# Optimization experiments

Hardware: AMD Instinct MI355X
Metric: run time of the kernel (lower is better)

Reference implementation:

```python
import jax, jax.numpy as jnp
import numpy as np

# Config matching init_kwargs
DIM = 768; NH = 12; K = 16; BASE_LR = 1.0  # mini_batch_size K, ttt_base_lr


def _ln(x, g, b, eps=1e-6):
    mu = x.mean(-1, keepdims=True)
    var = x.var(-1, keepdims=True)
    return g * (x - mu) * jax.lax.rsqrt(var + eps) + b


def _ln_l2_bwd(x, tgt, g, b, eps=1e-6):
    # grad wrt x of ||LN(x; g, b) - tgt||^2 (TTT fused layernorm-l2 backward)
    D = x.shape[-1]
    mu = x.mean(-1, keepdims=True)
    var = x.var(-1, keepdims=True)
    std = jnp.sqrt(var + eps)
    xh = (x - mu) / std
    gout = (g * xh + b) - tgt
    gxh = gout * g
    return (D * gxh - gxh.sum(-1, keepdims=True) - xh * (gxh * xh).sum(-1, keepdims=True)) / (D * std)


def _rotary(x, fc):
    # x: [..., N, hd]; fc: [N, hd//2] complex
    xr = x.reshape(*x.shape[:-1], -1, 2)
    xc = jax.lax.complex(xr[..., 0], xr[..., 1]) * fc
    return jnp.stack([jnp.real(xc), jnp.imag(xc)], -1).reshape(x.shape)


def setup_inputs() -> dict:
    key = jax.random.key(0)
    ks = jax.random.split(key, 6)
    B, N, C = 16, 1024, DIM
    nh2, hd, W2 = 2 * NH, C // NH, 2 * C
    f = jnp.float32
    x = jax.random.normal(ks[0], (B, N, C), f)
    qkv_w = jax.random.normal(ks[1], (C, 3 * C), f) * (1.0 / np.sqrt(C))
    proj_w = jax.random.normal(ks[2], (C, C), f) * (1.0 / np.sqrt(C))
    proj_b = jnp.zeros((C,), f)
    W1 = jax.random.normal(ks[3], (nh2, hd, hd), f) * 0.02  # per-head fast-weight init
    b1 = jnp.zeros((nh2, 1, hd), f)
    ttt_ln_w = jnp.ones((nh2, hd), f)
    ttt_ln_b = jnp.zeros((nh2, hd), f)
    post_ln_w = jnp.ones((W2,), f)
    post_ln_b = jnp.zeros((W2,), f)
    lr_w = jax.random.normal(ks[4], (W2, nh2), f) * 0.02  # learnable ttt lr projection
    lr_b = jnp.zeros((nh2,), f)
    token_idx_delta = jnp.zeros((K,), f)  # learnable token-idx offset, init 0
    return dict(x=x, qkv_w=qkv_w, proj_w=proj_w, proj_b=proj_b, W1=W1, b1=b1,
                ttt_ln_w=ttt_ln_w, ttt_ln_b=ttt_ln_b, post_ln_w=post_ln_w, post_ln_b=post_ln_b,
                lr_w=lr_w, lr_b=lr_b, token_idx_delta=token_idx_delta)


def reference(x, qkv_w, proj_w, proj_b, W1, b1, ttt_ln_w, ttt_ln_b,
              post_ln_w, post_ln_b, lr_w, lr_b, token_idx_delta):
    B, N, C = x.shape
    nh2, hd, W2 = 2 * NH, C // NH, 2 * C
    nmb = N // K
    # fused QKV projection (no bias)
    q, k, v = jnp.split(x @ qkv_w, 3, axis=-1)  # each [B,N,C]
    # bidirectional: concat forward stream with token-flipped backward stream
    qq = jnp.concatenate([q, jnp.flip(q, axis=-2)], axis=-1)  # [B,N,2C]
    kk = jnp.concatenate([k, jnp.flip(k, axis=-2)], axis=-1)
    vv = jnp.concatenate([v, jnp.flip(v, axis=-2)], axis=-1)
    xx = jnp.concatenate([x, jnp.flip(x, axis=-2)], axis=-1)

    def heads(t):  # [B,N,2C] -> [B,nh2,N,hd]
        return t.reshape(B, N, nh2, hd).transpose(0, 2, 1, 3)
    XQ, XK, XV = heads(qq), heads(kk), heads(vv)

    # rotary embedding with position_ids % mini_batch_size
    pos = (jnp.arange(N) % K).astype(jnp.float32)
    inv = 1.0 / (10000.0 ** (jnp.arange(0, hd, 2, dtype=jnp.float32) / hd))
    ang = pos[:, None] * inv[None, :]
    fc = jax.lax.complex(jnp.cos(ang), jnp.sin(ang))  # [N, hd//2]
    XQ = _rotary(XQ, fc)
    XK = _rotary(XK, fc)

    def mb(t):  # [B,nh2,N,hd] -> [B,nh2,nmb,K,hd]
        return t.reshape(B, nh2, nmb, K, hd)
    XQ, XK, XV = mb(XQ), mb(XK), mb(XV)

    # eta: token_idx (1/i, learnable offset, clipped) x per-token learnable lr
    Xr = xx.reshape(B, nmb, K, W2)
    lr = jax.nn.sigmoid(Xr @ lr_w + lr_b) * (BASE_LR / hd)  # [B,nmb,K,nh2]
    tok = jnp.clip(1.0 / jnp.arange(1, K + 1, dtype=jnp.float32) + token_idx_delta, 0.0)
    # eta[b,h,m,i,j] = tok[i] * lr[b,m,j,h]
    eta = tok[None, None, None, :, None] * lr.transpose(0, 3, 1, 2)[:, :, :, None, :]  # [B,nh2,nmb,K,K]

    mask = jnp.tril(jnp.ones((K, K), x.dtype))  # AR mask within mini-batch
    g = ttt_ln_w[None, :, None, :]   # [1,nh2,1,hd]
    bt = ttt_ln_b[None, :, None, :]
    W1_0 = jnp.broadcast_to(W1[None], (B, nh2, hd, hd))
    b1_0 = jnp.broadcast_to(b1[None], (B, nh2, 1, hd))

    def step(carry, inp):
        W, bb = carry
        xq, xk, xv, et = inp  # [B,nh2,K,hd] x3, [B,nh2,K,K]
        Z1 = xk @ W + bb
        grad = _ln_l2_bwd(Z1, xv - xk, g, bt)  # dl/dZ1
        attn = jnp.einsum('bhid,bhjd->bhij', xq, xk) * mask
        b1_bar = bb - (et * mask) @ grad
        Z1_bar = xq @ W - (et * attn) @ grad + b1_bar
        last = et[..., -1, :, None]  # eta row of last token [B,nh2,K,1]
        Wn = W - jnp.einsum('bhkd,bhke->bhde', last * xk, grad)
        bn = bb - (last * grad).sum(-2, keepdims=True)
        out = xq + _ln(Z1_bar, g, bt)  # residual + per-head TTT layernorm
        return (Wn, bn), out

    xs = (XQ.transpose(2, 0, 1, 3, 4), XK.transpose(2, 0, 1, 3, 4),
          XV.transpose(2, 0, 1, 3, 4), eta.transpose(2, 0, 1, 3, 4))
    _, Z = jax.lax.scan(step, (W1_0, b1_0), xs)  # Z: [nmb,B,nh2,K,hd]

    Z = Z.transpose(1, 2, 0, 3, 4).reshape(B, nh2, N, hd).transpose(0, 2, 1, 3).reshape(B, N, W2)
    Z = _ln(Z, post_ln_w, post_ln_b)  # mult_norm post-norm
    zf, zb = jnp.split(Z, 2, axis=-1)
    out = zf * jnp.flip(zb, axis=-2)  # merge forward / flipped-backward streams
    return out @ proj_w + proj_b
```

## Files before the change

kernel.cpp:

```cpp
#include <hip/hip_runtime.h>
#include <hip/hip_bf16.h>

#define Bq   16
#define Nseq 1024
#define Cdim 768
#define NH2  24
#define W2D  1536
#define KB   16
#define NMB  64

typedef short bfrag8 __attribute__((ext_vector_type(8)));
typedef short bfrag4 __attribute__((ext_vector_type(4)));
typedef float f32x4  __attribute__((ext_vector_type(4)));

__device__ __forceinline__ short f2bs(float x) {
  union { __hip_bfloat16 b; short s; } u;
  u.b = __float2bfloat16(x);
  return u.s;
}
__device__ __forceinline__ bfrag8 cvt8(const float* v) {
  bfrag8 r;
#pragma unroll
  for (int i = 0; i < 8; ++i) r[i] = f2bs(v[i]);
  return r;
}
__device__ __forceinline__ bfrag4 cvt4(float a, float b, float c, float d) {
  bfrag4 r;
  r[0] = f2bs(a); r[1] = f2bs(b); r[2] = f2bs(c); r[3] = f2bs(d);
  return r;
}
__device__ __forceinline__ void async_copy16(const void* g, void* l) {
  __builtin_amdgcn_global_load_lds((const __attribute__((address_space(1))) void*)g,
                                   (__attribute__((address_space(3))) void*)l, 16, 0, 0);
}

#if defined(__has_builtin)
#  if __has_builtin(__builtin_amdgcn_mfma_f32_16x16x16bf16_1k)
#    define HAVE_MFMA16X16X16 1
#  endif
#endif
__device__ __forceinline__ f32x4 mfma16(bfrag4 a, bfrag4 b, f32x4 c) {
#ifdef HAVE_MFMA16X16X16
  return __builtin_amdgcn_mfma_f32_16x16x16bf16_1k(a, b, c, 0, 0, 0);
#else
  f32x4 d;
  asm volatile("v_mfma_f32_16x16x16_bf16 %0, %1, %2, %3"
               : "=v"(d) : "v"(a), "v"(b), "v"(c));
  return d;
#endif
}

__device__ __forceinline__ void lds_fence() {
  asm volatile("s_waitcnt lgkmcnt(0)" ::: "memory");
  __builtin_amdgcn_sched_barrier(0);
}

template<int N>
__device__ __forceinline__ float dpp_ror(float x) {
  union { float f; int i; } a, r;
  a.f = x;
  r.i = __builtin_amdgcn_update_dpp(0, a.i, 0x120 | N, 0xF, 0xF, 1);
  return r.f;
}
__device__ __forceinline__ float rowsum16(float x) {
  x += dpp_ror<8>(x);
  x += dpp_ror<4>(x);
  x += dpp_ror<2>(x);
  x += dpp_ror<1>(x);
  return x;
}

__global__ __launch_bounds__(256) void gemm_bf16_kernel(
    const __hip_bfloat16* __restrict__ A,
    const __hip_bfloat16* __restrict__ Bt,
    const float* __restrict__ bias, float* __restrict__ C,
    int M, int Kd, int Nd, int gx)
{
  __shared__ short sA[128 * 64];
  __shared__ short sB[128 * 64];
  __shared__ float sEp[4][16 * 68];
  const int t = threadIdx.x;
  const int w = t >> 6, lane = t & 63;
  const int quad = lane >> 4, li = lane & 15;
  const int wm = w & 1, wn = w >> 1;

  const int nwg = gridDim.x;
  const int q8 = nwg >> 3;
  const int lid = ((int)blockIdx.x & 7) * q8 + ((int)blockIdx.x >> 3);
  const int m0 = (lid / gx) * 128, n0 = (lid % gx) * 128;

  f32x4 acc[4][4];
#pragma unroll
  for (int mt = 0; mt < 4; ++mt)
#pragma unroll
    for (int nt = 0; nt < 4; ++nt) acc[mt][nt] = (f32x4){0.f, 0.f, 0.f, 0.f};

  const __hip_bfloat16* Ab = A + (size_t)m0 * Kd;
  const __hip_bfloat16* Bb = Bt + (size_t)n0 * Kd;

#pragma unroll 1
  for (int k0 = 0; k0 < Kd; k0 += 64) {
    __syncthreads();
#pragma unroll
    for (int i = 0; i < 4; ++i) {
      int c = i * 256 + t;
      int row = c >> 3;
      int gl = (c & 7) ^ (row & 7);
      async_copy16(Ab + (size_t)row * Kd + k0 + gl * 8, &sA[c * 8]);
      async_copy16(Bb + (size_t)row * Kd + k0 + gl * 8, &sB[c * 8]);
    }
    __syncthreads();
#pragma unroll
    for (int ks = 0; ks < 2; ++ks) {
      bfrag8 aF[4], bF[4];
#pragma unroll
      for (int mt = 0; mt < 4; ++mt) {
        int row = wm * 64 + mt * 16 + li;
        int gi = (ks * 4 + quad) ^ (row & 7);
        aF[mt] = *(const bfrag8*)(&sA[row * 64 + gi * 8]);
      }
#pragma unroll
      for (int nt = 0; nt < 4; ++nt) {
        int row = wn * 64 + nt * 16 + li;
        int gi = (ks * 4 + quad) ^ (row & 7);
        bF[nt] = *(const bfrag8*)(&sB[row * 64 + gi * 8]);
      }
#pragma unroll
      for (int mt = 0; mt < 4; ++mt)
#pragma unroll
        for (int nt = 0; nt < 4; ++nt)
          acc[mt][nt] = __builtin_amdgcn_mfma_f32_16x16x32_bf16(aF[mt], bF[nt], acc[mt][nt], 0, 0, 0);
    }
  }

  float* ep = sEp[w];
  const int erow = lane >> 2, ecb = lane & 3;
#pragma unroll
  for (int mt = 0; mt < 4; ++mt) {
#pragma unroll
    for (int nt = 0; nt < 4; ++nt) {
      int ncol = n0 + wn * 64 + nt * 16 + li;
      float bv = bias ? bias[ncol] : 0.f;
#pragma unroll
      for (int r = 0; r < 4; ++r)
        ep[(quad * 4 + r) * 68 + nt * 16 + li] = acc[mt][nt][r] + bv;
    }
    lds_fence();
    {
      size_t rbase = (size_t)(m0 + wm * 64 + mt * 16 + erow) * Nd + n0 + wn * 64 + ecb * 16;
#pragma unroll
      for (int j = 0; j < 4; ++j) {
        f32x4 v = *(const f32x4*)(&ep[erow * 68 + ecb * 16 + 4 * j]);
        *(f32x4*)(&C[rbase + 4 * j]) = v;
      }
    }
    lds_fence();
  }
}

__global__ __launch_bounds__(256) void transpose_cast_kernel(
    const float* __restrict__ B, __hip_bfloat16* __restrict__ Bt, int Kd, int Nd)
{
  __shared__ float tl[64][65];
  int k0 = blockIdx.x * 64, n0 = blockIdx.y * 64;
  int tx = threadIdx.x & 63, ty = threadIdx.x >> 6;
#pragma unroll
  for (int i = 0; i < 16; ++i) {
    int k = ty + i * 4;
    tl[k][tx] = B[(size_t)(k0 + k) * Nd + n0 + tx];
  }
  __syncthreads();
#pragma unroll
  for (int i = 0; i < 16; ++i) {
    int n = ty + i * 4;
    Bt[(size_t)(n0 + n) * Kd + k0 + tx] = __float2bfloat16(tl[tx][n]);
  }
}

__global__ __launch_bounds__(64) void lrcast_kernel(
    const float* __restrict__ x, const float* __restrict__ lr_w,
    const float* __restrict__ lr_b, float* __restrict__ lrout,
    __hip_bfloat16* __restrict__ xbf)
{
  const int pair = blockIdx.x;
  const int b = pair >> 9, n = pair & 511;
  const size_t r1 = (size_t)b * Nseq + n;
  const size_t r2 = (size_t)b * Nseq + (Nseq - 1 - n);
  const int l = threadIdx.x;
  const float* x1 = x + r1 * Cdim;
  const float* x2 = x + r2 * Cdim;

  float a1[NH2], a2[NH2];
#pragma unroll
  for (int hh = 0; hh < NH2; ++hh) { a1[hh] = 0.f; a2[hh] = 0.f; }

#pragma unroll 1
  for (int i = 0; i < 12; ++i) {
    int c = l + 64 * i;
    float xv1 = x1[c];
    float xv2 = x2[c];
    ((short*)xbf)[r1 * Cdim + c] = f2bs(xv1);
    ((short*)xbf)[r2 * Cdim + c] = f2bs(xv2);
    const float4* wlo = (const float4*)(lr_w + (size_t)c * NH2);
    const float4* whi = (const float4*)(lr_w + (size_t)(Cdim + c) * NH2);
#pragma unroll
    for (int q4 = 0; q4 < 6; ++q4) {
      float4 wa = wlo[q4], wb = whi[q4];
      a1[q4 * 4 + 0] += xv1 * wa.x + xv2 * wb.x;
      a1[q4 * 4 + 1] += xv1 * wa.y + xv2 * wb.y;
      a1[q4 * 4 + 2] += xv1 * wa.z + xv2 * wb.z;
      a1[q4 * 4 + 3] += xv1 * wa.w + xv2 * wb.w;
      a2[q4 * 4 + 0] += xv2 * wa.x + xv1 * wb.x;
      a2[q4 * 4 + 1] += xv2 * wa.y + xv1 * wb.y;
      a2[q4 * 4 + 2] += xv2 * wa.z + xv1 * wb.z;
      a2[q4 * 4 + 3] += xv2 * wa.w + xv1 * wb.w;
    }
  }
#pragma unroll
  for (int hh = 0; hh < NH2; ++hh) {
    float s = rowsum16(a1[hh]);
    s += __shfl_xor(s, 16);
    s += __shfl_xor(s, 32);
    a1[hh] = s;
    float u = rowsum16(a2[hh]);
    u += __shfl_xor(u, 16);
    u += __shfl_xor(u, 32);
    a2[hh] = u;
  }
  float m1 = 0.f, m2 = 0.f;
#pragma unroll
  for (int hh = 0; hh < NH2; ++hh) {
    m1 = (l == hh) ? a1[hh] : m1;
    m2 = (l == hh) ? a2[hh] : m2;
  }
  if (l < NH2) {
    float v1 = m1 + lr_b[l];
    float v2 = m2 + lr_b[l];
    lrout[r1 * NH2 + l] = (1.f / (1.f + expf(-v1))) * (1.f / 64.f);
    lrout[r2 * NH2 + l] = (1.f / (1.f + expf(-v2))) * (1.f / 64.f);
  }
}

__global__ __launch_bounds__(64, 1) void ttt_scan_kernel(
    const float* __restrict__ qkv,
    const float* __restrict__ lrg,
    const float* __restrict__ W1,
    const float* __restrict__ b1g,
    const float* __restrict__ lnw,
    const float* __restrict__ lnb,
    const float* __restrict__ tid,
    float* __restrict__ Zout)
{
  __shared__ float sQ[16 * 68], sK[16 * 68], sV[16 * 68];

  const int l = threadIdx.x;
  const int quad = l >> 4, li = l & 15;
  const int bh = blockIdx.x, b = bh / NH2, h = bh % NH2;
  const int chan = (h < 12) ? h * 64 : (h - 12) * 64;
  const bool flip = (h >= 12);
  const int bN = b * Nseq;

  float Wf[4][4][4];
  bfrag4 wB[4][4];
#pragma unroll
  for (int t = 0; t < 4; ++t)
#pragma unroll
    for (int kk = 0; kk < 4; ++kk) {
#pragma unroll
      for (int j = 0; j < 4; ++j)
        Wf[t][kk][j] = W1[h * 4096 + (kk * 16 + quad * 4 + j) * 64 + t * 16 + li];
      wB[t][kk] = cvt4(Wf[t][kk][0], Wf[t][kk][1], Wf[t][kk][2], Wf[t][kk][3]);
    }
  float bC[4], gv[4], bt_[4];
#pragma unroll
  for (int t = 0; t < 4; ++t) {
    bC[t]  = b1g[h * 64 + t * 16 + li];
    gv[t]  = lnw[h * 64 + t * 16 + li];
    bt_[t] = lnb[h * 64 + t * 16 + li];
  }

  float tokL;
  {
    float tk = 1.f / (float)(li + 1) + tid[li];
    tokL = tk > 0.f ? tk : 0.f;
  }
  float t15 = 1.f / 16.f + tid[15];
  t15 = t15 > 0.f ? t15 : 0.f;

  float c8[8], s8[8];
  {
    int pos = l >> 2;
#pragma unroll
    for (int pl = 0; pl < 8; ++pl) {
      int p = (l & 3) * 8 + pl;
      float inv = __expf(-((float)(2 * p) * (1.f / 64.f)) * 9.210340371976184f);
      float a = (float)pos * inv;
      c8[pl] = cosf(a);
      s8[pl] = sinf(a);
    }
  }

  float4 pf[3][4];
  float pflr[4];
  {
    int nn = l >> 2;
    int grow = flip ? (bN + Nseq - 1 - nn) : (bN + nn);
#pragma unroll
    for (int a = 0; a < 3; ++a) {
      const float* bse = qkv + (size_t)grow * 2304 + chan + a * 768 + (l & 3) * 16;
#pragma unroll
      for (int i = 0; i < 4; ++i) pf[a][i] = ((const float4*)bse)[i];
    }
#pragma unroll
    for (int r = 0; r < 4; ++r)
      pflr[r] = lrg[(size_t)(bN + quad * 4 + r) * NH2 + h];
  }

#pragma unroll 1
  for (int m = 0; m < NMB; ++m) {
    const int n0 = m * KB;

#pragma unroll
    for (int a = 0; a < 3; ++a) {
      float v16[16];
      *(float4*)(v16)      = pf[a][0]; *(float4*)(v16 + 4)  = pf[a][1];
      *(float4*)(v16 + 8)  = pf[a][2]; *(float4*)(v16 + 12) = pf[a][3];
      if (a < 2) {
#pragma unroll
        for (int pl = 0; pl < 8; ++pl) {
          float e = v16[2 * pl], o = v16[2 * pl + 1];
          v16[2 * pl]     = e * c8[pl] - o * s8[pl];
          v16[2 * pl + 1] = o * c8[pl] + e * s8[pl];
        }
      }
      float* dst = (a == 0 ? sQ : (a == 1 ? sK : sV)) + (l >> 2) * 68 + (l & 3) * 16;
#pragma unroll
      for (int i = 0; i < 4; ++i) ((f32x4*)dst)[i] = *(f32x4*)(v16 + 4 * i);
    }
    float lr4[4];
#pragma unroll
    for (int r = 0; r < 4; ++r) lr4[r] = pflr[r];
    lds_fence();

    if (m < NMB - 1) {
      int nn = (m + 1) * KB + (l >> 2);
      int grow = flip ? (bN + Nseq - 1 - nn) : (bN + nn);
#pragma unroll
      for (int a = 0; a < 3; ++a) {
        const float* bse = qkv + (size_t)grow * 2304 + chan + a * 768 + (l & 3) * 16;
#pragma unroll
        for (int i = 0; i < 4; ++i) pf[a][i] = ((const float4*)bse)[i];
      }
#pragma unroll
      for (int r = 0; r < 4; ++r)
        pflr[r] = lrg[(size_t)(bN + (m + 1) * KB + quad * 4 + r) * NH2 + h];
    }

    bfrag4 aQ4[4], aK4[4];
#pragma unroll
    for (int kk = 0; kk < 4; ++kk) {
      f32x4 q4 = *(const f32x4*)(&sQ[li * 68 + kk * 16 + quad * 4]);
      f32x4 k4 = *(const f32x4*)(&sK[li * 68 + kk * 16 + quad * 4]);
      aQ4[kk] = cvt4(q4[0], q4[1], q4[2], q4[3]);
      aK4[kk] = cvt4(k4[0], k4[1], k4[2], k4[3]);
    }
    float kC[4][4], vC[4][4];
#pragma unroll
    for (int t = 0; t < 4; ++t)
#pragma unroll
      for (int r = 0; r < 4; ++r) {
        int off = (quad * 4 + r) * 68 + t * 16 + li;
        kC[t][r] = sK[off]; vC[t][r] = sV[off];
      }

    f32x4 accZ[4], accQ[4];
#pragma unroll
    for (int t = 0; t < 4; ++t) {
      accZ[t] = (f32x4){0.f, 0.f, 0.f, 0.f};
      accQ[t] = (f32x4){0.f, 0.f, 0.f, 0.f};
#pragma unroll
      for (int kk = 0; kk < 4; ++kk) {
        accZ[t] = mfma16(aK4[kk], wB[t][kk], accZ[t]);
        accQ[t] = mfma16(aQ4[kk], wB[t][kk], accQ[t]);
      }
    }
    f32x4 accAT = (f32x4){0.f, 0.f, 0.f, 0.f};
#pragma unroll
    for (int kk = 0; kk < 4; ++kk)
      accAT = mfma16(aK4[kk], aQ4[kk], accAT);

    bfrag4 aCoef;
    {
      float cf[4];
#pragma unroll
      for (int r = 0; r < 4; ++r) {
        int j = quad * 4 + r;
        cf[r] = (j <= li) ? (-tokL * (accAT[r] + 1.f)) : 0.f;
      }
      aCoef = cvt4(cf[0], cf[1], cf[2], cf[3]);
    }

    float gs[4][4];
#pragma unroll
    for (int r = 0; r < 4; ++r) {
      float zt[4], xht[4], gxht[4];
      float s1 = 0.f, s2 = 0.f;
#pragma unroll
      for (int t = 0; t < 4; ++t) {
        zt[t] = accZ[t][r] + bC[t];
        s1 += zt[t];
        s2 += zt[t] * zt[t];
      }
      s1 = rowsum16(s1);
      s2 = rowsum16(s2);
      float mu = s1 * 0.015625f;
      float var = s2 * 0.015625f - mu * mu;
      float rstd = rsqrtf(var + 1e-6f);
      float r1 = 0.f, r2 = 0.f;
#pragma unroll
      for (int t = 0; t < 4; ++t) {
        xht[t] = (zt[t] - mu) * rstd;
        float gout = gv[t] * xht[t] + bt_[t] - (vC[t][r] - kC[t][r]);
        gxht[t] = gout * gv[t];
        r1 += gxht[t];
        r2 += gxht[t] * xht[t];
      }
      r1 = rowsum16(r1);
      r2 = rowsum16(r2);
      float lrr = lr4[r];
#pragma unroll
      for (int t = 0; t < 4; ++t) {
        float gd = (64.f * gxht[t] - r1 - xht[t] * r2) * rstd * 0.015625f;
        gs[t][r] = lrr * gd;
      }
    }

    bfrag4 bGrad[4], aXk[4];
#pragma unroll
    for (int t = 0; t < 4; ++t) {
      bGrad[t] = cvt4(gs[t][0], gs[t][1], gs[t][2], gs[t][3]);
      aXk[t]   = cvt4(kC[t][0], kC[t][1], kC[t][2], kC[t][3]);
    }

    f32x4 zb[4];
#pragma unroll
    for (int t = 0; t < 4; ++t) {
      f32x4 acc = accQ[t];
#pragma unroll
      for (int r = 0; r < 4; ++r) acc[r] += bC[t];
      zb[t] = mfma16(aCoef, bGrad[t], acc);
    }
#pragma unroll
    for (int r = 0; r < 4; ++r) {
      float s1 = 0.f, s2 = 0.f;
#pragma unroll
      for (int t = 0; t < 4; ++t) { s1 += zb[t][r]; s2 += zb[t][r] * zb[t][r]; }
      s1 = rowsum16(s1);
      s2 = rowsum16(s2);
      float mu = s1 * 0.015625f;
      float var = s2 * 0.015625f - mu * mu;
      float rstd = rsqrtf(var + 1e-6f);
#pragma unroll
      for (int t = 0; t < 4; ++t) {
        float qv = sQ[(quad * 4 + r) * 68 + t * 16 + li];
        float outv = qv + gv[t] * (zb[t][r] - mu) * rstd + bt_[t];
        Zout[(size_t)(bN + n0 + quad * 4 + r) * W2D + h * 64 + t * 16 + li] = outv;
      }
    }

#pragma unroll
    for (int mt = 0; mt < 4; ++mt)
#pragma unroll
      for (int t = 0; t < 4; ++t) {
        f32x4 g = mfma16(aXk[mt], bGrad[t], (f32x4){0.f, 0.f, 0.f, 0.f});
#pragma unroll
        for (int r = 0; r < 4; ++r) Wf[t][mt][r] -= t15 * g[r];
        wB[t][mt] = cvt4(Wf[t][mt][0], Wf[t][mt][1], Wf[t][mt][2], Wf[t][mt][3]);
      }
#pragma unroll
    for (int t = 0; t < 4; ++t) {
      float g0 = gs[t][0] + gs[t][1] + gs[t][2] + gs[t][3];
      g0 += __shfl_xor(g0, 16);
      g0 += __shfl_xor(g0, 32);
      bC[t] -= t15 * g0;
    }
  }
}

__global__ __launch_bounds__(256) void postln_mult_kernel(
    const float* __restrict__ Z, const float* __restrict__ wv,
    const float* __restrict__ bb, __hip_bfloat16* __restrict__ hbuf)
{
  __shared__ float red[16];
  const int pair = blockIdx.x;
  const int b = pair >> 9, n = pair & 511;
  const size_t r1 = (size_t)b * Nseq + n;
  const size_t r2 = (size_t)b * Nseq + (Nseq - 1 - n);
  const float* z1 = Z + r1 * W2D;
  const float* z2 = Z + r2 * W2D;
  const int t = threadIdx.x;

  float v1[6], v2[6];
  float s1a = 0.f, s2a = 0.f, s1b = 0.f, s2b = 0.f;
#pragma unroll
  for (int r = 0; r < 6; ++r) {
    int c = t + 256 * r;
    float a = z1[c]; v1[r] = a; s1a += a; s2a += a * a;
    float d = z2[c]; v2[r] = d; s1b += d; s2b += d * d;
  }
#pragma unroll
  for (int o = 1; o < 64; o <<= 1) {
    s1a += __shfl_xor(s1a, o); s2a += __shfl_xor(s2a, o);
    s1b += __shfl_xor(s1b, o); s2b += __shfl_xor(s2b, o);
  }
  if ((t & 63) == 0) {
    int w = t >> 6;
    red[w] = s1a; red[4 + w] = s2a; red[8 + w] = s1b; red[12 + w] = s2b;
  }
  __syncthreads();
  s1a = red[0] + red[1] + red[2] + red[3];
  s2a = red[4] + red[5] + red[6] + red[7];
  s1b = red[8] + red[9] + red[10] + red[11];
  s2b = red[12] + red[13] + red[14] + red[15];
  float mu1 = s1a * (1.f / 1536.f);
  float var1 = s2a * (1.f / 1536.f) - mu1 * mu1;
  float rstd1 = rsqrtf(var1 + 1e-6f);
  float mu2 = s1b * (1.f / 1536.f);
  float var2 = s2b * (1.f / 1536.f) - mu2 * mu2;
  float rstd2 = rsqrtf(var2 + 1e-6f);
#pragma unroll
  for (int r = 0; r < 3; ++r) {
    int c = t + 256 * r;
    float a1  = wv[c] * (v1[r] - mu1) * rstd1 + bb[c];
    float a1b = wv[c + 768] * (v1[r + 3] - mu1) * rstd1 + bb[c + 768];
    float a2  = wv[c] * (v2[r] - mu2) * rstd2 + bb[c];
    float a2b = wv[c + 768] * (v2[r + 3] - mu2) * rstd2 + bb[c + 768];
    union { __hip_bfloat16 h; short s; } u1, u2;
    u1.h = __float2bfloat16(a1 * a2b);
    u2.h = __float2bfloat16(a2 * a1b);
    ((short*)hbuf)[r1 * Cdim + c] = u1.s;
    ((short*)hbuf)[r2 * Cdim + c] = u2.s;
  }
}

extern "C" void kernel_launch(void* const* d_in, const int* in_sizes, int n_in,
                              void* d_out, int out_size, void* d_ws, size_t ws_size,
                              hipStream_t stream)
{
  const float* x         = (const float*)d_in[0];
  const float* qkv_w     = (const float*)d_in[1];
  const float* proj_w    = (const float*)d_in[2];
  const float* proj_b    = (const float*)d_in[3];
  const float* W1        = (const float*)d_in[4];
  const float* b1        = (const float*)d_in[5];
  const float* ttt_ln_w  = (const float*)d_in[6];
  const float* ttt_ln_b  = (const float*)d_in[7];
  const float* post_ln_w = (const float*)d_in[8];
  const float* post_ln_b = (const float*)d_in[9];
  const float* lr_w      = (const float*)d_in[10];
  const float* lr_b      = (const float*)d_in[11];
  const float* tid       = (const float*)d_in[12];
  float* out = (float*)d_out;
  float* ws  = (float*)d_ws;

  float* qkv   = ws;
  float* lrbuf = ws + 37748736;
  float* Zbuf  = ws + 38141952;
  __hip_bfloat16* xbf    = (__hip_bfloat16*)(ws + 38141952);
  __hip_bfloat16* wqkv_t = (__hip_bfloat16*)(ws + 44433408);
  __hip_bfloat16* hbf    = (__hip_bfloat16*)(ws + 25165824);
  __hip_bfloat16* wproj_t= (__hip_bfloat16*)(ws + 37748736);

  const int Mrows = Bq * Nseq;

  {
    dim3 g(Cdim / 64, 3 * Cdim / 64);
    transpose_cast_kernel<<<g, 256, 0, stream>>>(qkv_w, wqkv_t, Cdim, 3 * Cdim);
  }
  lrcast_kernel<<<Mrows / 2, 64, 0, stream>>>(x, lr_w, lr_b, lrbuf, xbf);
  {
    int gx = 3 * Cdim / 128;
    int nwg = gx * (Mrows / 128);
    gemm_bf16_kernel<<<nwg, 256, 0, stream>>>(xbf, wqkv_t, nullptr, qkv, Mrows, Cdim, 3 * Cdim, gx);
  }

  ttt_scan_kernel<<<Bq * NH2, 64, 0, stream>>>(qkv, lrbuf, W1, b1, ttt_ln_w, ttt_ln_b, tid, Zbuf);

  postln_mult_kernel<<<Bq * Nseq / 2, 256, 0, stream>>>(Zbuf, post_ln_w, post_ln_b, hbf);
  {
    dim3 g(Cdim / 64, Cdim / 64);
    transpose_cast_kernel<<<g, 256, 0, stream>>>(proj_w, wproj_t, Cdim, Cdim);
  }
  {
    int gx = Cdim / 128;
    int nwg = gx * (Mrows / 128);
    gemm_bf16_kernel<<<nwg, 256, 0, stream>>>(hbf, wproj_t, proj_b, out, Mrows, Cdim, Cdim, gx);
  }
}
```

Before: 520.7 us.

## Double-buffer LDS staging of Q/K/V in TTT scan with two-step-ahead prefetch

Shared-memory Q/K/V tiles are double-buffered. The next mini-batch's rotary-transformed data is staged into the alternate buffer during the current step, and the global loads are issued two steps ahead. The aim is to take the staging and the LDS fence off the critical path at the start of each serial scan iteration and to give global loads more time to land. The cost is twice the LDS footprint and more live registers during the compute phase, which could add register pressure in a kernel with one wave per block.

Result: no change. 521.5 us (+0.2%).

```diff
diff --git a/kernel.cpp b/kernel.cpp
--- a/kernel.cpp
+++ b/kernel.cpp
@@ -251,7 +251,7 @@
     const float* __restrict__ tid,
     float* __restrict__ Zout)
 {
-  __shared__ float sQ[16 * 68], sK[16 * 68], sV[16 * 68];
+  __shared__ float sQ[2][16 * 68], sK[2][16 * 68], sV[2][16 * 68];
 
   const int l = threadIdx.x;
   const int quad = l >> 4, li = l & 15;
@@ -259,6 +259,7 @@
   const int chan = (h < 12) ? h * 64 : (h - 12) * 64;
   const bool flip = (h >= 12);
   const int bN = b * Nseq;
+  const int stok = l >> 2, sc0 = (l & 3) * 16;
 
   float Wf[4][4][4];
   bfrag4 wB[4][4];
@@ -289,37 +290,30 @@
 
   float c8[8], s8[8];
   {
-    int pos = l >> 2;
 #pragma unroll
     for (int pl = 0; pl < 8; ++pl) {
       int p = (l & 3) * 8 + pl;
       float inv = __expf(-((float)(2 * p) * (1.f / 64.f)) * 9.210340371976184f);
-      float a = (float)pos * inv;
+      float a = (float)stok * inv;
       c8[pl] = cosf(a);
       s8[pl] = sinf(a);
     }
   }
 
   float4 pf[3][4];
-  float pflr[4];
-  {
-    int nn = l >> 2;
+  float lrcur[4], pfl[4];
+
+  auto issue_qkv = [&](int mt) {
+    int nn = mt * KB + stok;
     int grow = flip ? (bN + Nseq - 1 - nn) : (bN + nn);
 #pragma unroll
     for (int a = 0; a < 3; ++a) {
-      const float* bse = qkv + (size_t)grow * 2304 + chan + a * 768 + (l & 3) * 16;
+      const float* bse = qkv + (size_t)grow * 2304 + chan + a * 768 + sc0;
 #pragma unroll
       for (int i = 0; i < 4; ++i) pf[a][i] = ((const float4*)bse)[i];
     }
-#pragma unroll
-    for (int r = 0; r < 4; ++r)
-      pflr[r] = lrg[(size_t)(bN + quad * 4 + r) * NH2 + h];
-  }
-
-#pragma unroll 1
-  for (int m = 0; m < NMB; ++m) {
-    const int n0 = m * KB;
-
+  };
+  auto stage = [&](int buf) {
 #pragma unroll
     for (int a = 0; a < 3; ++a) {
       float v16[16];
@@ -333,34 +327,31 @@
           v16[2 * pl + 1] = o * c8[pl] + e * s8[pl];
         }
       }
-      float* dst = (a == 0 ? sQ : (a == 1 ? sK : sV)) + (l >> 2) * 68 + (l & 3) * 16;
+      float* dst = (a == 0 ? sQ[buf] : (a == 1 ? sK[buf] : sV[buf])) + stok * 68 + sc0;
 #pragma unroll
       for (int i = 0; i < 4; ++i) ((f32x4*)dst)[i] = *(f32x4*)(v16 + 4 * i);
     }
-    float lr4[4];
-#pragma unroll
-    for (int r = 0; r < 4; ++r) lr4[r] = pflr[r];
-    lds_fence();
-
-    if (m < NMB - 1) {
-      int nn = (m + 1) * KB + (l >> 2);
-      int grow = flip ? (bN + Nseq - 1 - nn) : (bN + nn);
-#pragma unroll
-      for (int a = 0; a < 3; ++a) {
-        const float* bse = qkv + (size_t)grow * 2304 + chan + a * 768 + (l & 3) * 16;
-#pragma unroll
-        for (int i = 0; i < 4; ++i) pf[a][i] = ((const float4*)bse)[i];
-      }
-#pragma unroll
-      for (int r = 0; r < 4; ++r)
-        pflr[r] = lrg[(size_t)(bN + (m + 1) * KB + quad * 4 + r) * NH2 + h];
-    }
+  };
+
+  issue_qkv(0);
+#pragma unroll
+  for (int r = 0; r < 4; ++r) lrcur[r] = lrg[(size_t)(bN + quad * 4 + r) * NH2 + h];
+  stage(0);
+  issue_qkv(1);
+#pragma unroll
+  for (int r = 0; r < 4; ++r) pfl[r] = lrg[(size_t)(bN + KB + quad * 4 + r) * NH2 + h];
+  lds_fence();
+
+#pragma unroll 1
+  for (int m = 0; m < NMB; ++m) {
+    const int n0 = m * KB;
+    const int cur = m & 1, alt = cur ^ 1;
 
     bfrag4 aQ4[4], aK4[4];
 #pragma unroll
     for (int kk = 0; kk < 4; ++kk) {
-      f32x4 q4 = *(const f32x4*)(&sQ[li * 68 + kk * 16 + quad * 4]);
-      f32x4 k4 = *(const f32x4*)(&sK[li * 68 + kk * 16 + quad * 4]);
+      f32x4 q4 = *(const f32x4*)(&sQ[cur][li * 68 + kk * 16 + quad * 4]);
+      f32x4 k4 = *(const f32x4*)(&sK[cur][li * 68 + kk * 16 + quad * 4]);
       aQ4[kk] = cvt4(q4[0], q4[1], q4[2], q4[3]);
       aK4[kk] = cvt4(k4[0], k4[1], k4[2], k4[3]);
     }
@@ -370,8 +361,23 @@
 #pragma unroll
       for (int r = 0; r < 4; ++r) {
         int off = (quad * 4 + r) * 68 + t * 16 + li;
-        kC[t][r] = sK[off]; vC[t][r] = sV[off];
-      }
+        kC[t][r] = sK[cur][off]; vC[t][r] = sV[cur][off];
+      }
+    float lr4[4];
+#pragma unroll
+    for (int r = 0; r < 4; ++r) lr4[r] = lrcur[r];
+
+    if (m < NMB - 1) {
+      stage(alt);
+#pragma unroll
+      for (int r = 0; r < 4; ++r) lrcur[r] = pfl[r];
+      if (m < NMB - 2) {
+        issue_qkv(m + 2);
+#pragma unroll
+        for (int r = 0; r < 4; ++r)
+          pfl[r] = lrg[(size_t)(bN + (m + 2) * KB + quad * 4 + r) * NH2 + h];
+      }
+    }
 
     f32x4 accZ[4], accQ[4];
 #pragma unroll
@@ -462,7 +468,7 @@
       float rstd = rsqrtf(var + 1e-6f);
 #pragma unroll
       for (int t = 0; t < 4; ++t) {
-        float qv = sQ[(quad * 4 + r) * 68 + t * 16 + li];
+        float qv = sQ[cur][(quad * 4 + r) * 68 + t * 16 + li];
         float outv = qv + gv[t] * (zb[t][r] - mu) * rstd + bt_[t];
         Zout[(size_t)(bN + n0 + quad * 4 + r) * W2D + h * 64 + t * 16 + li] = outv;
       }
@@ -484,6 +490,8 @@
       g0 += __shfl_xor(g0, 32);
       bC[t] -= t15 * g0;
     }
+
+    lds_fence();
   }
 }
 
```
